# Kernel optimization log

Hardware: AMD Instinct MI355X
Metric: run time of the kernel (lower is better)

Reference implementation:

```python
import jax, jax.numpy as jnp
import numpy as np

B, I, H = 256, 512, 512


def _lin_init(k, out_dim, in_dim):
    bound = 1.0 / np.sqrt(in_dim)
    kw, kb = jax.random.split(k)
    W = jax.random.uniform(kw, (out_dim, in_dim), minval=-bound, maxval=bound, dtype=jnp.float32)
    b = jax.random.uniform(kb, (out_dim,), minval=-bound, maxval=bound, dtype=jnp.float32)
    return W, b


def setup_inputs() -> dict:
    key = jax.random.key(0)
    ks = jax.random.split(key, 16)
    inp = {}
    inp['inputs'] = jax.random.normal(ks[0], (B, I), dtype=jnp.float32)
    inp['h0'] = jax.random.normal(ks[1], (B, H), dtype=jnp.float32) * 0.1
    inp['c0'] = jax.random.normal(ks[2], (B, H), dtype=jnp.float32) * 0.1
    inp['hebb'] = jax.random.uniform(ks[3], (B, H, H), minval=-0.01, maxval=0.01, dtype=jnp.float32)
    # plastic recurrent weights: w = 0.02*rand - 0.01, alpha = 1e-4*rand
    inp['w'] = 0.02 * jax.random.uniform(ks[4], (H, H), dtype=jnp.float32) - 0.01
    inp['alpha'] = 1e-4 * jax.random.uniform(ks[5], (1, 1, H), dtype=jnp.float32)
    inp['Wxf'], inp['bxf'] = _lin_init(ks[6], H, I)
    inp['Whf'], inp['bhf'] = _lin_init(ks[7], H, H)
    inp['Wxi'], inp['bxi'] = _lin_init(ks[8], H, I)
    inp['Whi'], inp['bhi'] = _lin_init(ks[9], H, H)
    inp['Wxo'], inp['bxo'] = _lin_init(ks[10], H, I)
    inp['Who'], inp['bho'] = _lin_init(ks[11], H, H)
    inp['Wxc'], inp['bxc'] = _lin_init(ks[12], H, I)
    inp['Wmod'], inp['bmod'] = _lin_init(ks[13], 1, H)   # h2mod: H -> 1
    inp['Wfan'], inp['bfan'] = _lin_init(ks[14], H, 1)   # modfanout: 1 -> H
    return inp


def reference(inputs, h0, c0, hebb, w, alpha,
              Wxf, bxf, Whf, bhf, Wxi, bxi, Whi, bhi,
              Wxo, bxo, Who, bho, Wxc, bxc, Wmod, bmod, Wfan, bfan):
    # gates (torch Linear: y = x @ W.T + b)
    fgt = jax.nn.sigmoid(inputs @ Wxf.T + bxf + h0 @ Whf.T + bhf)
    ipt = jax.nn.sigmoid(inputs @ Wxi.T + bxi + h0 @ Whi.T + bhi)
    opt = jax.nn.sigmoid(inputs @ Wxo.T + bxo + h0 @ Who.T + bho)
    # plastic recurrent path: h0 @ (w + alpha * hebb), per-sample fast weights
    h2c = jnp.einsum('bh,bhk->bk', h0, w + alpha * hebb)
    inputstocell = jnp.tanh(inputs @ Wxc.T + bxc + h2c)
    cell = fgt * c0 + ipt * inputstocell
    hactiv = opt * jnp.tanh(cell)
    # Hebbian outer-product trace update with neuromodulated learning rate
    deltahebb = jnp.einsum('bh,bk->bhk', h0, inputstocell)  # [B,H,H]
    myeta = jnp.tanh(hactiv @ Wmod.T + bmod)                # [B,1]
    myeta = myeta * Wfan[:, 0][None, :] + bfan              # modfanout(1->H): [B,H]
    hebb_new = jnp.clip(hebb + myeta[:, None, :] * deltahebb, -2.0, 2.0)
    return hactiv, cell, hebb_new
```

## Files before the change

### kernel.cpp

```cpp
#include <hip/hip_runtime.h>
#include <math.h>

#define B_ 256
#define I_ 512
#define H_ 512
#define BH (B_*H_)
#define NCH 8
#define HCH (H_/NCH)

typedef float f4v __attribute__((ext_vector_type(4)));


#define TK 32
#define LDB 34
#define TILE_F (TK*LDB)
#define NGEMM 1024

__global__ __launch_bounds__(256) void k_dot_gates(
    const float* __restrict__ hebb, const float* __restrict__ h0,
    const float* __restrict__ inputs,
    const float* __restrict__ Wxf, const float* __restrict__ Whf,
    const float* __restrict__ Wxi, const float* __restrict__ Whi,
    const float* __restrict__ Wxo, const float* __restrict__ Who,
    const float* __restrict__ Wxc, const float* __restrict__ w,
    float* __restrict__ pre, float* __restrict__ part) {

    __shared__ float smem[4 * TILE_F];
    int bid = blockIdx.x;
    int tid = threadIdx.x;

    if (bid < NGEMM) {
        int ks = bid & 1;
        int m0 = ((bid >> 1) & 7) * 32;
        int n0 = (bid >> 4) * 32;
        int g  = n0 >> 9;
        int ko0 = n0 & 511;

        const float* Asrc = ks ? h0 : inputs;
        const float* Bsrc;
        bool wpath = false;
        if (ks == 0) {
            Bsrc = (g == 0) ? Wxf : (g == 1) ? Wxi : (g == 2) ? Wxo : Wxc;
        } else {
            if (g == 3) { Bsrc = w; wpath = true; }
            else Bsrc = (g == 0) ? Whf : (g == 1) ? Whi : Who;
        }

        int row = tid >> 3;
        int c4  = tid & 7;
        int tx  = tid & 15, ty = tid >> 4;

        float acc[2][2] = {{0.f, 0.f}, {0.f, 0.f}};
        float4 areg, breg;

        auto LOAD = [&](int t) {
            int kb = t * TK;
            areg = *(const float4*)&Asrc[(size_t)(m0 + row) * 512 + kb + c4 * 4];
            if (wpath)
                breg = *(const float4*)&Bsrc[(size_t)(kb + row) * 512 + ko0 + c4 * 4];
            else
                breg = *(const float4*)&Bsrc[(size_t)(ko0 + row) * 512 + kb + c4 * 4];
        };
        auto STORE = [&](int pbuf) {
            float* As = smem + pbuf * 2 * TILE_F;
            float* Bs = As + TILE_F;
            #pragma unroll
            for (int j = 0; j < 4; ++j)
                As[(c4 * 4 + j) * LDB + row] = ((const float*)&areg)[j];
            if (wpath) {
                #pragma unroll
                for (int j = 0; j < 4; ++j)
                    Bs[row * LDB + c4 * 4 + j] = ((const float*)&breg)[j];
            } else {
                #pragma unroll
                for (int j = 0; j < 4; ++j)
                    Bs[(c4 * 4 + j) * LDB + row] = ((const float*)&breg)[j];
            }
        };

        LOAD(0);
        STORE(0);
        for (int t = 0; t < 16; ++t) {
            __syncthreads();
            if (t < 15) LOAD(t + 1);
            int pb = t & 1;
            const float* As = smem + pb * 2 * TILE_F;
            const float* Bs = As + TILE_F;
            #pragma unroll
            for (int kk = 0; kk < TK; ++kk) {
                float2 a2 = *(const float2*)&As[kk * LDB + ty * 2];
                float2 b2 = *(const float2*)&Bs[kk * LDB + tx * 2];
                acc[0][0] += a2.x * b2.x; acc[0][1] += a2.x * b2.y;
                acc[1][0] += a2.y * b2.x; acc[1][1] += a2.y * b2.y;
            }
            if (t < 15) STORE(pb ^ 1);
        }

        float* pb_out = pre + (size_t)(ks * 4 + g) * BH;
        #pragma unroll
        for (int i = 0; i < 2; ++i) {
            #pragma unroll
            for (int j = 0; j < 2; ++j) {
                int bnum = m0 + ty * 2 + i;
                int ko = ko0 + tx * 2 + j;
                pb_out[(size_t)bnum * H_ + ko] = acc[i][j];
            }
        }
    } else {
        int hbid = bid - NGEMM;
        int b  = hbid >> 3;
        int ch = hbid & 7;

        float*  h0s = smem;
        float4* red = (float4*)(smem + 64);

        if (tid < HCH) h0s[tid] = h0[b * H_ + ch * HCH + tid];
        __syncthreads();

        const float4* hbp = (const float4*)(hebb + ((size_t)b * H_ + (size_t)ch * HCH) * H_);
        int tk = tid & 127;
        int th = tid >> 7;
        float4 acc = make_float4(0.f, 0.f, 0.f, 0.f);
        #pragma unroll 8
        for (int r = 0; r < 32; ++r) {
            int hh = th * 32 + r;
            float s = h0s[hh];
            float4 vv = hbp[(size_t)hh * 128 + tk];
            acc.x += s * vv.x; acc.y += s * vv.y;
            acc.z += s * vv.z; acc.w += s * vv.w;
        }
        red[tid] = acc;
        __syncthreads();
        if (tid < 128) {
            float4 a = red[tid], c = red[tid + 128];
            float4 o = make_float4(a.x + c.x, a.y + c.y, a.z + c.z, a.w + c.w);
            ((float4*)(part + ((size_t)ch * B_ + b) * H_))[tid] = o;
        }
    }
}

__global__ __launch_bounds__(256) void k_finalize(
    const float* __restrict__ pre, const float* __restrict__ part,
    const float* __restrict__ c0, const float* __restrict__ alpha,
    const float* __restrict__ bxf, const float* __restrict__ bhf,
    const float* __restrict__ bxi, const float* __restrict__ bhi,
    const float* __restrict__ bxo, const float* __restrict__ bho,
    const float* __restrict__ bxc,
    const float* __restrict__ Wmod, const float* __restrict__ bmod,
    const float* __restrict__ Wfan, const float* __restrict__ bfan,
    float* __restrict__ out, float* __restrict__ v) {

    int b = blockIdx.x;
    int t = threadIdx.x;

    float c2r[2];
    float local = 0.f;
    #pragma unroll
    for (int s = 0; s < 2; ++s) {
        int k = t + s * 256;
        float dot = 0.f;
        #pragma unroll
        for (int c = 0; c < NCH; ++c) dot += part[((size_t)c * B_ + b) * H_ + k];
        size_t off = (size_t)b * H_ + k;
        float pf = pre[0 * BH + off] + pre[4 * BH + off] + bxf[k] + bhf[k];
        float pi = pre[1 * BH + off] + pre[5 * BH + off] + bxi[k] + bhi[k];
        float po = pre[2 * BH + off] + pre[6 * BH + off] + bxo[k] + bho[k];
        float pc = pre[3 * BH + off] + pre[7 * BH + off] + bxc[k];
        float c2 = tanhf(pc + alpha[k] * dot);
        float fg = 1.f / (1.f + expf(-pf));
        float ig = 1.f / (1.f + expf(-pi));
        float og = 1.f / (1.f + expf(-po));
        float cell = fg * c0[off] + ig * c2;
        float ha = og * tanhf(cell);
        out[off] = ha;
        out[BH + off] = cell;
        c2r[s] = c2;
        local += ha * Wmod[k];
    }
    float x = local;
    #pragma unroll
    for (int off = 32; off > 0; off >>= 1) x += __shfl_down(x, off, 64);
    __shared__ float red[4];
    int wid = t >> 6, lane = t & 63;
    if (lane == 0) red[wid] = x;
    __syncthreads();
    float s4 = red[0] + red[1] + red[2] + red[3];
    float myeta = tanhf(s4 + bmod[0]);
    #pragma unroll
    for (int s = 0; s < 2; ++s) {
        int k = t + s * 256;
        v[(size_t)b * H_ + k] = (myeta * Wfan[k] + bfan[k]) * c2r[s];
    }
}

__global__ __launch_bounds__(256) void k_update(
    const float4* __restrict__ hebb, const float* __restrict__ h0,
    const float* __restrict__ v, float* __restrict__ out) {
    const int total = B_ * H_ * (H_ / 4);
    int stride = gridDim.x * blockDim.x;
    int base = blockIdx.x * blockDim.x + threadIdx.x;
    for (int f = total - stride + base; f >= 0; f -= stride) {
        int k4 = f & 127;
        int h  = (f >> 7) & 511;
        int b  = f >> 16;
        float u = h0[(b << 9) + h];
        const float4* vv4 = (const float4*)v;
        float4 vv = vv4[(b << 7) + k4];
        float4 hb = hebb[f];
        f4v r;
        r.x = fminf(fmaxf(hb.x + u * vv.x, -2.f), 2.f);
        r.y = fminf(fmaxf(hb.y + u * vv.y, -2.f), 2.f);
        r.z = fminf(fmaxf(hb.z + u * vv.z, -2.f), 2.f);
        r.w = fminf(fmaxf(hb.w + u * vv.w, -2.f), 2.f);
        __builtin_nontemporal_store(r, (f4v*)(out) + f);
    }
}

extern "C" void kernel_launch(void* const* d_in, const int* in_sizes, int n_in,
                              void* d_out, int out_size, void* d_ws, size_t ws_size,
                              hipStream_t stream) {
    const float* inputs = (const float*)d_in[0];
    const float* h0     = (const float*)d_in[1];
    const float* c0     = (const float*)d_in[2];
    const float* hebb   = (const float*)d_in[3];
    const float* w      = (const float*)d_in[4];
    const float* alpha  = (const float*)d_in[5];
    const float* Wxf = (const float*)d_in[6];  const float* bxf = (const float*)d_in[7];
    const float* Whf = (const float*)d_in[8];  const float* bhf = (const float*)d_in[9];
    const float* Wxi = (const float*)d_in[10]; const float* bxi = (const float*)d_in[11];
    const float* Whi = (const float*)d_in[12]; const float* bhi = (const float*)d_in[13];
    const float* Wxo = (const float*)d_in[14]; const float* bxo = (const float*)d_in[15];
    const float* Who = (const float*)d_in[16]; const float* bho = (const float*)d_in[17];
    const float* Wxc = (const float*)d_in[18]; const float* bxc = (const float*)d_in[19];
    const float* Wmod = (const float*)d_in[20]; const float* bmod = (const float*)d_in[21];
    const float* Wfan = (const float*)d_in[22]; const float* bfan = (const float*)d_in[23];

    float* out = (float*)d_out;
    float* ws  = (float*)d_ws;
    float* pre  = ws;
    float* part = ws + 8 * BH;
    float* vbuf = ws + 16 * BH;

    k_dot_gates<<<NGEMM + B_ * NCH, 256, 0, stream>>>(
        hebb, h0, inputs,
        Wxf, Whf, Wxi, Whi, Wxo, Who, Wxc, w, pre, part);
    k_finalize<<<B_, 256, 0, stream>>>(pre, part, c0, alpha,
                                       bxf, bhf, bxi, bhi, bxo, bho, bxc,
                                       Wmod, bmod, Wfan, bfan, out, vbuf);
    k_update<<<2048, 256, 0, stream>>>((const float4*)hebb, h0, vbuf,
                                       out + 2 * BH);
}
```

Baseline: 171.6 us.

## Move per-sample hebb dot into finalize kernel, split gate GEMM out

The per-sample h0·hebb reduction moves out of the combined GEMM kernel and into the finalize kernel. That kernel now runs 512 threads per batch row, reduces over the full H dimension in shared memory, and then applies the gate nonlinearities. This removes the 'part' workspace round trip and the 8-way partial sum reads. The cost is that the 256MB-class hebb stream now runs with only 256 blocks in a separate kernel, after the GEMM instead of concurrently with it, which may reduce memory parallelism.

```diff
diff --git a/kernel.cpp b/kernel.cpp
--- a/kernel.cpp
+++ b/kernel.cpp
@@ -5,8 +5,6 @@
 #define I_ 512
 #define H_ 512
 #define BH (B_*H_)
-#define NCH 8
-#define HCH (H_/NCH)
 
 typedef float f4v __attribute__((ext_vector_type(4)));
 
@@ -16,132 +14,100 @@
 #define TILE_F (TK*LDB)
 #define NGEMM 1024
 
-__global__ __launch_bounds__(256) void k_dot_gates(
-    const float* __restrict__ hebb, const float* __restrict__ h0,
-    const float* __restrict__ inputs,
+__global__ __launch_bounds__(256) void k_gates(
+    const float* __restrict__ h0, const float* __restrict__ inputs,
     const float* __restrict__ Wxf, const float* __restrict__ Whf,
     const float* __restrict__ Wxi, const float* __restrict__ Whi,
     const float* __restrict__ Wxo, const float* __restrict__ Who,
     const float* __restrict__ Wxc, const float* __restrict__ w,
-    float* __restrict__ pre, float* __restrict__ part) {
+    float* __restrict__ pre) {
 
     __shared__ float smem[4 * TILE_F];
     int bid = blockIdx.x;
     int tid = threadIdx.x;
 
-    if (bid < NGEMM) {
-        int ks = bid & 1;
-        int m0 = ((bid >> 1) & 7) * 32;
-        int n0 = (bid >> 4) * 32;
-        int g  = n0 >> 9;
-        int ko0 = n0 & 511;
-
-        const float* Asrc = ks ? h0 : inputs;
-        const float* Bsrc;
-        bool wpath = false;
-        if (ks == 0) {
-            Bsrc = (g == 0) ? Wxf : (g == 1) ? Wxi : (g == 2) ? Wxo : Wxc;
-        } else {
-            if (g == 3) { Bsrc = w; wpath = true; }
-            else Bsrc = (g == 0) ? Whf : (g == 1) ? Whi : Who;
-        }
-
-        int row = tid >> 3;
-        int c4  = tid & 7;
-        int tx  = tid & 15, ty = tid >> 4;
-
-        float acc[2][2] = {{0.f, 0.f}, {0.f, 0.f}};
-        float4 areg, breg;
-
-        auto LOAD = [&](int t) {
-            int kb = t * TK;
-            areg = *(const float4*)&Asrc[(size_t)(m0 + row) * 512 + kb + c4 * 4];
-            if (wpath)
-                breg = *(const float4*)&Bsrc[(size_t)(kb + row) * 512 + ko0 + c4 * 4];
-            else
-                breg = *(const float4*)&Bsrc[(size_t)(ko0 + row) * 512 + kb + c4 * 4];
-        };
-        auto STORE = [&](int pbuf) {
-            float* As = smem + pbuf * 2 * TILE_F;
-            float* Bs = As + TILE_F;
+    int ks = bid & 1;
+    int m0 = ((bid >> 1) & 7) * 32;
+    int n0 = (bid >> 4) * 32;
+    int g  = n0 >> 9;
+    int ko0 = n0 & 511;
+
+    const float* Asrc = ks ? h0 : inputs;
+    const float* Bsrc;
+    bool wpath = false;
+    if (ks == 0) {
+        Bsrc = (g == 0) ? Wxf : (g == 1) ? Wxi : (g == 2) ? Wxo : Wxc;
+    } else {
+        if (g == 3) { Bsrc = w; wpath = true; }
+        else Bsrc = (g == 0) ? Whf : (g == 1) ? Whi : Who;
+    }
+
+    int row = tid >> 3;
+    int c4  = tid & 7;
+    int tx  = tid & 15, ty = tid >> 4;
+
+    float acc[2][2] = {{0.f, 0.f}, {0.f, 0.f}};
+    float4 areg, breg;
+
+    auto LOAD = [&](int t) {
+        int kb = t * TK;
+        areg = *(const float4*)&Asrc[(size_t)(m0 + row) * 512 + kb + c4 * 4];
+        if (wpath)
+            breg = *(const float4*)&Bsrc[(size_t)(kb + row) * 512 + ko0 + c4 * 4];
+        else
+            breg = *(const float4*)&Bsrc[(size_t)(ko0 + row) * 512 + kb + c4 * 4];
+    };
+    auto STORE = [&](int pbuf) {
+        float* As = smem + pbuf * 2 * TILE_F;
+        float* Bs = As + TILE_F;
+        #pragma unroll
+        for (int j = 0; j < 4; ++j)
+            As[(c4 * 4 + j) * LDB + row] = ((const float*)&areg)[j];
+        if (wpath) {
             #pragma unroll
             for (int j = 0; j < 4; ++j)
-                As[(c4 * 4 + j) * LDB + row] = ((const float*)&areg)[j];
-            if (wpath) {
-                #pragma unroll
-                for (int j = 0; j < 4; ++j)
-                    Bs[row * LDB + c4 * 4 + j] = ((const float*)&breg)[j];
-            } else {
-                #pragma unroll
-                for (int j = 0; j < 4; ++j)
-                    Bs[(c4 * 4 + j) * LDB + row] = ((const float*)&breg)[j];
-            }
-        };
-
-        LOAD(0);
-        STORE(0);
-        for (int t = 0; t < 16; ++t) {
-            __syncthreads();
-            if (t < 15) LOAD(t + 1);
-            int pb = t & 1;
-            const float* As = smem + pb * 2 * TILE_F;
-            const float* Bs = As + TILE_F;
+                Bs[row * LDB + c4 * 4 + j] = ((const float*)&breg)[j];
+        } else {
             #pragma unroll
-            for (int kk = 0; kk < TK; ++kk) {
-                float2 a2 = *(const float2*)&As[kk * LDB + ty * 2];
-                float2 b2 = *(const float2*)&Bs[kk * LDB + tx * 2];
-                acc[0][0] += a2.x * b2.x; acc[0][1] += a2.x * b2.y;
-                acc[1][0] += a2.y * b2.x; acc[1][1] += a2.y * b2.y;
-            }
-            if (t < 15) STORE(pb ^ 1);
+            for (int j = 0; j < 4; ++j)
+                Bs[(c4 * 4 + j) * LDB + row] = ((const float*)&breg)[j];
         }
-
-        float* pb_out = pre + (size_t)(ks * 4 + g) * BH;
+    };
+
+    LOAD(0);
+    STORE(0);
+    for (int t = 0; t < 16; ++t) {
+        __syncthreads();
+        if (t < 15) LOAD(t + 1);
+        int pb = t & 1;
+        const float* As = smem + pb * 2 * TILE_F;
+        const float* Bs = As + TILE_F;
         #pragma unroll
-        for (int i = 0; i < 2; ++i) {
-            #pragma unroll
-            for (int j = 0; j < 2; ++j) {
-                int bnum = m0 + ty * 2 + i;
-                int ko = ko0 + tx * 2 + j;
-                pb_out[(size_t)bnum * H_ + ko] = acc[i][j];
-            }
+        for (int kk = 0; kk < TK; ++kk) {
+            float2 a2 = *(const float2*)&As[kk * LDB + ty * 2];
+            float2 b2 = *(const float2*)&Bs[kk * LDB + tx * 2];
+            acc[0][0] += a2.x * b2.x; acc[0][1] += a2.x * b2.y;
+            acc[1][0] += a2.y * b2.x; acc[1][1] += a2.y * b2.y;
         }
-    } else {
-        int hbid = bid - NGEMM;
-        int b  = hbid >> 3;
-        int ch = hbid & 7;
-
-        float*  h0s = smem;
-        float4* red = (float4*)(smem + 64);
-
-        if (tid < HCH) h0s[tid] = h0[b * H_ + ch * HCH + tid];
-        __syncthreads();
-
-        const float4* hbp = (const float4*)(hebb + ((size_t)b * H_ + (size_t)ch * HCH) * H_);
-        int tk = tid & 127;
-        int th = tid >> 7;
-        float4 acc = make_float4(0.f, 0.f, 0.f, 0.f);
-        #pragma unroll 8
-        for (int r = 0; r < 32; ++r) {
-            int hh = th * 32 + r;
-            float s = h0s[hh];
-            float4 vv = hbp[(size_t)hh * 128 + tk];
-            acc.x += s * vv.x; acc.y += s * vv.y;
-            acc.z += s * vv.z; acc.w += s * vv.w;
+        if (t < 15) STORE(pb ^ 1);
+    }
+
+    float* pb_out = pre + (size_t)(ks * 4 + g) * BH;
+    #pragma unroll
+    for (int i = 0; i < 2; ++i) {
+        #pragma unroll
+        for (int j = 0; j < 2; ++j) {
+            int bnum = m0 + ty * 2 + i;
+            int ko = ko0 + tx * 2 + j;
+            pb_out[(size_t)bnum * H_ + ko] = acc[i][j];
         }
-        red[tid] = acc;
-        __syncthreads();
-        if (tid < 128) {
-            float4 a = red[tid], c = red[tid + 128];
-            float4 o = make_float4(a.x + c.x, a.y + c.y, a.z + c.z, a.w + c.w);
-            ((float4*)(part + ((size_t)ch * B_ + b) * H_))[tid] = o;
-        }
-    }
-}
-
-__global__ __launch_bounds__(256) void k_finalize(
-    const float* __restrict__ pre, const float* __restrict__ part,
-    const float* __restrict__ c0, const float* __restrict__ alpha,
+    }
+}
+
+__global__ __launch_bounds__(512) void k_dotfin(
+    const float* __restrict__ hebb, const float* __restrict__ h0,
+    const float* __restrict__ pre, const float* __restrict__ c0,
+    const float* __restrict__ alpha,
     const float* __restrict__ bxf, const float* __restrict__ bhf,
     const float* __restrict__ bxi, const float* __restrict__ bhi,
     const float* __restrict__ bxo, const float* __restrict__ bho,
@@ -150,47 +116,57 @@
     const float* __restrict__ Wfan, const float* __restrict__ bfan,
     float* __restrict__ out, float* __restrict__ v) {
 
+    __shared__ float h0s[H_];
+    __shared__ float plds[4 * H_];
+    __shared__ float red[8];
+
     int b = blockIdx.x;
     int t = threadIdx.x;
 
-    float c2r[2];
-    float local = 0.f;
+    h0s[t & 511] = h0[(size_t)b * H_ + (t & 511)];
+    __syncthreads();
+
+    int hg = t >> 7;
+    int k4 = t & 127;
+    const float4* hb4 = (const float4*)hebb + ((size_t)b << 16);
+    float4 acc = make_float4(0.f, 0.f, 0.f, 0.f);
+    #pragma unroll 8
+    for (int r = 0; r < 128; ++r) {
+        int h = (hg << 7) + r;
+        float s = h0s[h];
+        float4 vv = hb4[(size_t)h * 128 + k4];
+        acc.x += s * vv.x; acc.y += s * vv.y;
+        acc.z += s * vv.z; acc.w += s * vv.w;
+    }
+    ((float4*)plds)[hg * 128 + k4] = acc;
+    __syncthreads();
+
+    int k = t;
+    float dot = plds[k] + plds[H_ + k] + plds[2 * H_ + k] + plds[3 * H_ + k];
+    size_t off = (size_t)b * H_ + k;
+    float pf = pre[0 * BH + off] + pre[4 * BH + off] + bxf[k] + bhf[k];
+    float pi = pre[1 * BH + off] + pre[5 * BH + off] + bxi[k] + bhi[k];
+    float po = pre[2 * BH + off] + pre[6 * BH + off] + bxo[k] + bho[k];
+    float pc = pre[3 * BH + off] + pre[7 * BH + off] + bxc[k];
+    float c2 = tanhf(pc + alpha[k] * dot);
+    float fg = 1.f / (1.f + expf(-pf));
+    float ig = 1.f / (1.f + expf(-pi));
+    float og = 1.f / (1.f + expf(-po));
+    float cell = fg * c0[off] + ig * c2;
+    float ha = og * tanhf(cell);
+    out[off] = ha;
+    out[BH + off] = cell;
+
+    float x = ha * Wmod[k];
     #pragma unroll
-    for (int s = 0; s < 2; ++s) {
-        int k = t + s * 256;
-        float dot = 0.f;
-        #pragma unroll
-        for (int c = 0; c < NCH; ++c) dot += part[((size_t)c * B_ + b) * H_ + k];
-        size_t off = (size_t)b * H_ + k;
-        float pf = pre[0 * BH + off] + pre[4 * BH + off] + bxf[k] + bhf[k];
-        float pi = pre[1 * BH + off] + pre[5 * BH + off] + bxi[k] + bhi[k];
-        float po = pre[2 * BH + off] + pre[6 * BH + off] + bxo[k] + bho[k];
-        float pc = pre[3 * BH + off] + pre[7 * BH + off] + bxc[k];
-        float c2 = tanhf(pc + alpha[k] * dot);
-        float fg = 1.f / (1.f + expf(-pf));
-        float ig = 1.f / (1.f + expf(-pi));
-        float og = 1.f / (1.f + expf(-po));
-        float cell = fg * c0[off] + ig * c2;
-        float ha = og * tanhf(cell);
-        out[off] = ha;
-        out[BH + off] = cell;
-        c2r[s] = c2;
-        local += ha * Wmod[k];
-    }
-    float x = local;
-    #pragma unroll
-    for (int off = 32; off > 0; off >>= 1) x += __shfl_down(x, off, 64);
-    __shared__ float red[4];
+    for (int o = 32; o > 0; o >>= 1) x += __shfl_down(x, o, 64);
     int wid = t >> 6, lane = t & 63;
     if (lane == 0) red[wid] = x;
     __syncthreads();
-    float s4 = red[0] + red[1] + red[2] + red[3];
-    float myeta = tanhf(s4 + bmod[0]);
-    #pragma unroll
-    for (int s = 0; s < 2; ++s) {
-        int k = t + s * 256;
-        v[(size_t)b * H_ + k] = (myeta * Wfan[k] + bfan[k]) * c2r[s];
-    }
+    float s8 = red[0] + red[1] + red[2] + red[3]
+             + red[4] + red[5] + red[6] + red[7];
+    float myeta = tanhf(s8 + bmod[0]);
+    v[off] = (myeta * Wfan[k] + bfan[k]) * c2;
 }
 
 __global__ __launch_bounds__(256) void k_update(
@@ -238,15 +214,13 @@
     float* out = (float*)d_out;
     float* ws  = (float*)d_ws;
     float* pre  = ws;
-    float* part = ws + 8 * BH;
-    float* vbuf = ws + 16 * BH;
-
-    k_dot_gates<<<NGEMM + B_ * NCH, 256, 0, stream>>>(
-        hebb, h0, inputs,
-        Wxf, Whf, Wxi, Whi, Wxo, Who, Wxc, w, pre, part);
-    k_finalize<<<B_, 256, 0, stream>>>(pre, part, c0, alpha,
-                                       bxf, bhf, bxi, bhi, bxo, bho, bxc,
-                                       Wmod, bmod, Wfan, bfan, out, vbuf);
+    float* vbuf = ws + 8 * BH;
+
+    k_gates<<<NGEMM, 256, 0, stream>>>(h0, inputs,
+        Wxf, Whf, Wxi, Whi, Wxo, Who, Wxc, w, pre);
+    k_dotfin<<<B_, 512, 0, stream>>>(hebb, h0, pre, c0, alpha,
+        bxf, bhf, bxi, bhi, bxo, bho, bxc,
+        Wmod, bmod, Wfan, bfan, out, vbuf);
     k_update<<<2048, 256, 0, stream>>>((const float4*)hebb, h0, vbuf,
                                        out + 2 * BH);
 }
```

Measured after the change: 189.5 us. 10.4% more time.

## Fuse finalize into hebb update kernel, recomputing gates per row chunk

Applied to the files above, without the earlier changes.

Merges the per-batch finalize kernel into the Hebbian update kernel. Each of 2048 blocks recomputes the gate activations and the modulation vector for its batch row and keeps v in shared memory, then updates a 64-row chunk of hebb. This removes one kernel launch and the round trip of the v buffer through global memory. In exchange, the gate and reduction work is repeated eight times per batch row, and the reversed block order is meant to reuse hebb data still in cache from the previous kernel.

```diff
diff --git a/kernel.cpp b/kernel.cpp
--- a/kernel.cpp
+++ b/kernel.cpp
@@ -139,22 +139,29 @@
     }
 }
 
-__global__ __launch_bounds__(256) void k_finalize(
+__global__ __launch_bounds__(256) void k_updatev(
+    const float* __restrict__ hebb, const float* __restrict__ h0,
     const float* __restrict__ pre, const float* __restrict__ part,
-    const float* __restrict__ c0, const float* __restrict__ alpha,
+    const float* __restrict__ c0in, const float* __restrict__ alpha,
     const float* __restrict__ bxf, const float* __restrict__ bhf,
     const float* __restrict__ bxi, const float* __restrict__ bhi,
     const float* __restrict__ bxo, const float* __restrict__ bho,
     const float* __restrict__ bxc,
     const float* __restrict__ Wmod, const float* __restrict__ bmod,
     const float* __restrict__ Wfan, const float* __restrict__ bfan,
-    float* __restrict__ out, float* __restrict__ v) {
-
-    int b = blockIdx.x;
-    int t = threadIdx.x;
-
-    float c2r[2];
-    float local = 0.f;
+    float* __restrict__ out) {
+
+    __shared__ float vsh[512] __attribute__((aligned(16)));
+    __shared__ float h0s[64];
+    __shared__ float red[4];
+    __shared__ float myeta_sh;
+
+    int rb = 2047 - (int)blockIdx.x;
+    int b  = rb >> 3;
+    int ch = rb & 7;
+    int t  = threadIdx.x;
+
+    float c2r[2], ep = 0.f;
     #pragma unroll
     for (int s = 0; s < 2; ++s) {
         int k = t + s * 256;
@@ -170,49 +177,48 @@
         float fg = 1.f / (1.f + expf(-pf));
         float ig = 1.f / (1.f + expf(-pi));
         float og = 1.f / (1.f + expf(-po));
-        float cell = fg * c0[off] + ig * c2;
+        float cell = fg * c0in[off] + ig * c2;
         float ha = og * tanhf(cell);
-        out[off] = ha;
-        out[BH + off] = cell;
+        if (ch == 0) {
+            out[off] = ha;
+            out[BH + off] = cell;
+        }
         c2r[s] = c2;
-        local += ha * Wmod[k];
-    }
-    float x = local;
+        ep += ha * Wmod[k];
+    }
     #pragma unroll
-    for (int off = 32; off > 0; off >>= 1) x += __shfl_down(x, off, 64);
-    __shared__ float red[4];
+    for (int o = 32; o > 0; o >>= 1) ep += __shfl_down(ep, o, 64);
     int wid = t >> 6, lane = t & 63;
-    if (lane == 0) red[wid] = x;
+    if (lane == 0) red[wid] = ep;
+    if (t < 64) h0s[t] = h0[(size_t)b * H_ + ch * 64 + t];
     __syncthreads();
-    float s4 = red[0] + red[1] + red[2] + red[3];
-    float myeta = tanhf(s4 + bmod[0]);
+    if (t == 0)
+        myeta_sh = tanhf(red[0] + red[1] + red[2] + red[3] + bmod[0]);
+    __syncthreads();
+    float myeta = myeta_sh;
     #pragma unroll
     for (int s = 0; s < 2; ++s) {
         int k = t + s * 256;
-        v[(size_t)b * H_ + k] = (myeta * Wfan[k] + bfan[k]) * c2r[s];
-    }
-}
-
-__global__ __launch_bounds__(256) void k_update(
-    const float4* __restrict__ hebb, const float* __restrict__ h0,
-    const float* __restrict__ v, float* __restrict__ out) {
-    const int total = B_ * H_ * (H_ / 4);
-    int stride = gridDim.x * blockDim.x;
-    int base = blockIdx.x * blockDim.x + threadIdx.x;
-    for (int f = total - stride + base; f >= 0; f -= stride) {
-        int k4 = f & 127;
-        int h  = (f >> 7) & 511;
-        int b  = f >> 16;
-        float u = h0[(b << 9) + h];
-        const float4* vv4 = (const float4*)v;
-        float4 vv = vv4[(b << 7) + k4];
-        float4 hb = hebb[f];
+        vsh[k] = (myeta * Wfan[k] + bfan[k]) * c2r[s];
+    }
+    __syncthreads();
+
+    int c4 = t & 127;
+    int rg = t >> 7;
+    const float4* gin  = (const float4*)(hebb + (size_t)(b * H_ + ch * 64) * H_) + c4;
+    f4v*          gout = (f4v*)(out + 2 * BH + (size_t)(b * H_ + ch * 64) * H_) + c4;
+    f4v vq = *(const f4v*)&vsh[c4 * 4];
+    #pragma unroll 8
+    for (int i = 0; i < 32; ++i) {
+        int row = i * 2 + rg;
+        float u = h0s[row];
+        float4 hb4 = gin[(size_t)row * 128];
         f4v r;
-        r.x = fminf(fmaxf(hb.x + u * vv.x, -2.f), 2.f);
-        r.y = fminf(fmaxf(hb.y + u * vv.y, -2.f), 2.f);
-        r.z = fminf(fmaxf(hb.z + u * vv.z, -2.f), 2.f);
-        r.w = fminf(fmaxf(hb.w + u * vv.w, -2.f), 2.f);
-        __builtin_nontemporal_store(r, (f4v*)(out) + f);
+        r.x = fminf(fmaxf(hb4.x + u * vq.x, -2.f), 2.f);
+        r.y = fminf(fmaxf(hb4.y + u * vq.y, -2.f), 2.f);
+        r.z = fminf(fmaxf(hb4.z + u * vq.z, -2.f), 2.f);
+        r.w = fminf(fmaxf(hb4.w + u * vq.w, -2.f), 2.f);
+        __builtin_nontemporal_store(r, gout + (size_t)row * 128);
     }
 }
 
@@ -239,14 +245,12 @@
     float* ws  = (float*)d_ws;
     float* pre  = ws;
     float* part = ws + 8 * BH;
-    float* vbuf = ws + 16 * BH;
 
     k_dot_gates<<<NGEMM + B_ * NCH, 256, 0, stream>>>(
         hebb, h0, inputs,
         Wxf, Whf, Wxi, Whi, Wxo, Who, Wxc, w, pre, part);
-    k_finalize<<<B_, 256, 0, stream>>>(pre, part, c0, alpha,
-                                       bxf, bhf, bxi, bhi, bxo, bho, bxc,
-                                       Wmod, bmod, Wfan, bfan, out, vbuf);
-    k_update<<<2048, 256, 0, stream>>>((const float4*)hebb, h0, vbuf,
-                                       out + 2 * BH);
+    k_updatev<<<2048, 256, 0, stream>>>(
+        hebb, h0, pre, part, c0, alpha,
+        bxf, bhf, bxi, bhi, bxo, bho, bxc,
+        Wmod, bmod, Wfan, bfan, out);
 }
```

After: 161.0 us. 6.2% less time.
